# Kernel optimization log

Hardware: AMD Instinct MI355X
Metric: run time of the kernel (lower is better)

## Reference

```python
import jax, jax.numpy as jnp
import numpy as np

DIS_NORM = 6.0 * 512 / 1000.0  # 6 * D(z=0) * Nmesh / Boxsize with D(0)=1


def setup_inputs() -> dict:
    key = jax.random.key(0)
    x = jax.random.normal(key, (2, 4, 128, 128, 128), dtype=jnp.float32)
    return {"x": x}


def _lag2eul(x):
    N, C = x.shape[0], x.shape[1]
    D, H, W = x.shape[2], x.shape[3], x.shape[4]
    P = D * H * W
    Cout = C - 3 if C > 3 else 1

    # rm_dis_mean=True: mean displacement, detached
    dis_mean = jax.lax.stop_gradient(jnp.mean(x[:, :3], axis=(2, 3, 4), keepdims=True))

    pos = (x[:, :3] - dis_mean) * DIS_NORM  # (N,3,D,H,W)
    gd = jnp.arange(D, dtype=x.dtype) + 0.5
    gh = jnp.arange(H, dtype=x.dtype) + 0.5
    gw = jnp.arange(W, dtype=x.dtype) + 0.5
    grid = jnp.stack(jnp.meshgrid(gd, gh, gw, indexing='ij'))  # (3,D,H,W)
    pos = (pos + grid[None]).reshape(N, 3, P)

    if C > 3:
        val = x[:, 3:].reshape(N, Cout, P)
    else:
        val = jnp.ones((N, Cout, P), dtype=x.dtype)

    intpos = jnp.floor(pos).astype(jnp.int32)
    # 8 trilinear neighbors: bit b of n -> offset along dim b
    neighbors = (jnp.arange(8, dtype=jnp.int32)[None, :] >> jnp.arange(3, dtype=jnp.int32)[:, None]) & 1  # (3,8)
    tgt = intpos[:, :, :, None] + neighbors[None, :, None, :]  # (N,3,P,8)

    kernel = jnp.prod(1.0 - jnp.abs(pos[:, :, :, None] - tgt.astype(x.dtype)), axis=1)  # (N,P,8)
    src = val[:, :, :, None] * kernel[:, None, :, :]  # (N,Cout,P,8)

    # periodic=False: mask out-of-bounds deposits
    bounds = jnp.array([D, H, W], dtype=jnp.int32)[None, :, None, None]
    mask = jnp.all((tgt >= 0) & (tgt < bounds), axis=1)  # (N,P,8)
    ind = (tgt[:, 0] * H + tgt[:, 1]) * W + tgt[:, 2]  # (N,P,8)
    ind = jnp.clip(ind, 0, P - 1)
    src = jnp.where(mask[:, None, :, :], src, jnp.zeros((), dtype=x.dtype))

    def scatter_one(ind_n, src_n):
        mesh = jnp.zeros((Cout, P), dtype=src_n.dtype)
        return mesh.at[:, ind_n.reshape(-1)].add(src_n.reshape(Cout, -1))

    mesh = jax.vmap(scatter_one)(ind, src)  # (N,Cout,P)
    return mesh.reshape(N, Cout, D, H, W)


def reference(x):
    return _lag2eul(x)
```

## Files before the change

### kernel.cpp

```cpp
#include <hip/hip_runtime.h>

#define NBATCH 2
#define NDIM   128
#define NP     (128 * 128 * 128)
#define DIS_NORM 3.072f

#define TS   16
#define LO   5
#define HI   6
#define WIN  (TS + LO + HI)
#define WIN2 (WIN * WIN)
#define WINF (WIN * WIN * WIN)
#define TPB  8
#define NTILE (TPB * TPB * TPB)
#define NTHR 512

#define FXSCALE 16777216.0f
#define FXINV   (1.0f / 16777216.0f)

#define SLAB 19696

#define SUMS_OFF 0
#define SLABS_OFF 1024
#define WS_FLOATS ((size_t)SLABS_OFF + (size_t)NBATCH * NTILE * SLAB)
#define WS_NEEDED_BYTES (WS_FLOATS * sizeof(float))

__device__ __constant__ int BASE27[27] = {
    0,216,792,972,1548,3084,3564,3744,4224,
    4376,4952,6488,6968,8504,12600,13880,14360,15640,
    16040,16220,16700,16852,17332,18612,19012,19164,19564};

__global__ __launch_bounds__(256) void prep_kernel(const float* __restrict__ x,
                                                   float* __restrict__ ws,
                                                   float* __restrict__ out) {
    const int plane = blockIdx.y;
    if (plane < 6) {
        const int n = plane / 3, c = plane % 3;
        const float4* xp = (const float4*)(x + ((size_t)n * 4 + c) * NP);
        float s = 0.0f;
        for (int i = blockIdx.x * 256 + threadIdx.x; i < NP / 4; i += 128 * 256) {
            float4 v = xp[i];
            s += (v.x + v.y) + (v.z + v.w);
        }
        #pragma unroll
        for (int off = 32; off > 0; off >>= 1) s += __shfl_down(s, off, 64);
        __shared__ float wsum[4];
        if ((threadIdx.x & 63) == 0) wsum[threadIdx.x >> 6] = s;
        __syncthreads();
        if (threadIdx.x == 0)
            ws[SUMS_OFF + plane * 128 + blockIdx.x] =
                (wsum[0] + wsum[1]) + (wsum[2] + wsum[3]);
    } else {
        float4* o4 = (float4*)out;
        const float4 z = make_float4(0.f, 0.f, 0.f, 0.f);
        for (int i = blockIdx.x * 256 + threadIdx.x; i < NBATCH * NP / 4; i += 128 * 256)
            o4[i] = z;
    }
}

__device__ __forceinline__ void load_means128(const float* __restrict__ ws, int n,
                                              float& m0, float& m1, float& m2) {
    float s0 = 0.f, s1 = 0.f, s2 = 0.f;
    const float* p0 = ws + SUMS_OFF + (n * 3 + 0) * 128;
    const float* p1 = ws + SUMS_OFF + (n * 3 + 1) * 128;
    const float* p2 = ws + SUMS_OFF + (n * 3 + 2) * 128;
    #pragma unroll 4
    for (int b = 0; b < 128; ++b) { s0 += p0[b]; s1 += p1[b]; s2 += p2[b]; }
    const float inv_np = 1.0f / (float)NP;
    m0 = s0 * inv_np; m1 = s1 * inv_np; m2 = s2 * inv_np;
}

__device__ __forceinline__ void deposit_pair(unsigned long long* __restrict__ winU,
                                             int b, float va, float vb) {
    const int fa = __float2int_rn(va * FXSCALE);
    const int fb = __float2int_rn(vb * FXSCALE);
    const bool odd = (b & 1);
    const long long packed = (((long long)fb) << 32) + (long long)fa;
    const long long hiOnly = ((long long)fa) << 32;
    atomicAdd(&winU[b >> 1], (unsigned long long)(odd ? hiOnly : packed));
    if (odd) atomicAdd(&winU[(b >> 1) + 1], (unsigned long long)(long long)fb);
}

__global__ __launch_bounds__(NTHR, 4) void scatter_tile_kernel(
        const float* __restrict__ x, const float* __restrict__ ws,
        float* __restrict__ slabs, float* __restrict__ out) {
    const int blk = blockIdx.x;
    const int n = blk >> 9;
    const int t = blk & (NTILE - 1);
    const int tx = t & 7, ty = (t >> 3) & 7, tz = t >> 6;

    __shared__ ulonglong2 win2[(WINF + 3) / 4 + 1];
    unsigned long long* winU = (unsigned long long*)win2;
    {
        float4* z4 = (float4*)win2;
        const float4 z = make_float4(0.f, 0.f, 0.f, 0.f);
        for (int i = threadIdx.x; i < (WINF + 3) / 4 + 1; i += NTHR) z4[i] = z;
    }
    float m0, m1, m2;
    load_means128(ws, n, m0, m1, m2);
    __syncthreads();

    const int i0 = threadIdx.x * 8;
    const int lw0 = i0 & 15;
    const int lh  = (i0 >> 4) & 15;
    const int ld  = i0 >> 8;
    const int gd = tz * TS + ld, gh = ty * TS + lh, gw0 = tx * TS + lw0;
    const size_t prow = ((size_t)gd * NDIM + gh) * NDIM + gw0;

    const float4* x4 = (const float4*)(x + (size_t)n * 4 * NP);
    const size_t q = prow >> 2;
    const size_t s4 = NP / 4;
    float4 a0 = x4[0 * s4 + q], a1 = x4[0 * s4 + q + 1];
    float4 b0 = x4[1 * s4 + q], b1 = x4[1 * s4 + q + 1];
    float4 c0 = x4[2 * s4 + q], c1 = x4[2 * s4 + q + 1];
    float4 e0 = x4[3 * s4 + q], e1 = x4[3 * s4 + q + 1];
    const float D0[8] = {a0.x, a0.y, a0.z, a0.w, a1.x, a1.y, a1.z, a1.w};
    const float D1[8] = {b0.x, b0.y, b0.z, b0.w, b1.x, b1.y, b1.z, b1.w};
    const float D2[8] = {c0.x, c0.y, c0.z, c0.w, c1.x, c1.y, c1.z, c1.w};
    const float VV[8] = {e0.x, e0.y, e0.z, e0.w, e1.x, e1.y, e1.z, e1.w};

    const int od = tz * TS - LO, oh = ty * TS - LO, ow = tx * TS - LO;
    float* sp = out + (size_t)n * NP;

    #pragma unroll
    for (int k = 0; k < 8; ++k) {
        const float pd = (D0[k] - m0) * DIS_NORM + (float)gd + 0.5f;
        const float ph = (D1[k] - m1) * DIS_NORM + (float)gh + 0.5f;
        const float pw = (D2[k] - m2) * DIS_NORM + (float)(gw0 + k) + 0.5f;
        const float v = VV[k];

        const float fd = floorf(pd), fh = floorf(ph), fw = floorf(pw);
        const int id = (int)fd, ih = (int)fh, iw = (int)fw;
        const float rd = pd - fd, rh = ph - fh, rw = pw - fw;

        const int wd = id - od, wh = ih - oh, ww = iw - ow;
        if ((unsigned)wd <= WIN - 2 && (unsigned)wh <= WIN - 2 &&
            (unsigned)ww <= WIN - 2) {
            const int b00 = (wd * WIN + wh) * WIN + ww;
            const float sd0 = v * (1.0f - rd), sd1 = v * rd;
            const float h0 = 1.0f - rh, h1 = rh;
            const float q0 = 1.0f - rw, q1 = rw;
            deposit_pair(winU, b00,              sd0 * h0 * q0, sd0 * h0 * q1);
            deposit_pair(winU, b00 + WIN,        sd0 * h1 * q0, sd0 * h1 * q1);
            deposit_pair(winU, b00 + WIN2,       sd1 * h0 * q0, sd1 * h0 * q1);
            deposit_pair(winU, b00 + WIN2 + WIN, sd1 * h1 * q0, sd1 * h1 * q1);
        } else {
            const float wd2[2]  = {1.0f - rd, rd};
            const float wh2[2]  = {1.0f - rh, rh};
            const float ww2[2]  = {1.0f - rw, rw};
            #pragma unroll
            for (int dd = 0; dd < 2; ++dd) {
                const int td = id + dd, wdc = wd + dd;
                const bool dW = (unsigned)wdc < WIN, dM = (unsigned)td < NDIM;
                if (!dM && !dW) continue;
                #pragma unroll
                for (int hh = 0; hh < 2; ++hh) {
                    const int th = ih + hh, whc = wh + hh;
                    const bool hW = (unsigned)whc < WIN, hM = (unsigned)th < NDIM;
                    const float vdh = v * wd2[dd] * wh2[hh];
                    #pragma unroll
                    for (int wi = 0; wi < 2; ++wi) {
                        const int tw = iw + wi, wwc = ww + wi;
                        const bool wW = (unsigned)wwc < WIN, wM = (unsigned)tw < NDIM;
                        const float dep = vdh * ww2[wi];
                        if (dW && hW && wW) {
                            const int cb = (wdc * WIN + whc) * WIN + wwc;
                            const int fx = __float2int_rn(dep * FXSCALE);
                            const long long cv = (cb & 1)
                                ? (((long long)fx) << 32) : (long long)fx;
                            atomicAdd(&winU[cb >> 1], (unsigned long long)cv);
                        } else if (dM && hM && wM) {
                            atomicAdd(sp + ((size_t)td * NDIM + th) * NDIM + tw, dep);
                        }
                    }
                }
            }
        }
    }

    __syncthreads();

    {
        const int NU = (WINF + 1) / 2;
        for (int i = threadIdx.x; i < NU; i += NTHR) {
            const unsigned long long u = winU[i];
            const int lo = (int)(unsigned)(u & 0xffffffffull);
            const int hi = (int)(u >> 32) + (lo < 0 ? 1 : 0);
            float2 f;
            f.x = (float)lo * FXINV;
            f.y = (float)hi * FXINV;
            ((float2*)winU)[i] = f;
        }
    }
    __syncthreads();
    const float* winF = (const float*)winU;

    const int EXTY[3] = {6, 16, 5};
    const int nbase = n << 9;
    for (int r = threadIdx.x; r < WIN2; r += NTHR) {
        const int lz = r / WIN;
        const int ly = r - lz * WIN;
        int mz, pz;
        if (lz < LO) { mz = -1; pz = lz; }
        else if (lz < LO + TS) { mz = 0; pz = lz - LO; }
        else { mz = 1; pz = lz - LO - TS; }
        int my, py;
        if (ly < LO) { my = -1; py = ly; }
        else if (ly < LO + TS) { my = 0; py = ly - LO; }
        else { my = 1; py = ly - LO - TS; }
        const int dtz = tz + mz, dty = ty + my;
        if ((unsigned)dtz >= TPB || (unsigned)dty >= TPB) continue;

        const int jz = 1 - mz, jy = 1 - my;
        const int ey = EXTY[jy];
        const int rowoff = pz * ey + py;
        const int pobase = jz * 9 + jy * 3;
        const float* src = winF + r * WIN;
        const int slabRow = nbase + (dtz * 8 + dty) * 8;

        if (tx > 0) {
            float* d = slabs + (size_t)(slabRow + tx - 1) * SLAB
                     + BASE27[pobase + 2] + rowoff * 5;
            #pragma unroll
            for (int k = 0; k < 5; ++k) d[k] = src[k];
        }
        {
            float* d = slabs + (size_t)(slabRow + tx) * SLAB
                     + BASE27[pobase + 1] + rowoff * 16;
            #pragma unroll
            for (int k = 0; k < 4; ++k) {
                float4 v;
                v.x = src[5 + 4 * k]; v.y = src[6 + 4 * k];
                v.z = src[7 + 4 * k]; v.w = src[8 + 4 * k];
                ((float4*)d)[k] = v;
            }
        }
        if (tx < TPB - 1) {
            float* d = slabs + (size_t)(slabRow + tx + 1) * SLAB
                     + BASE27[pobase + 0] + rowoff * 6;
            #pragma unroll
            for (int k = 0; k < 6; ++k) d[k] = src[21 + k];
        }
    }
}

__global__ __launch_bounds__(NTHR) void gather_tile_kernel(const float* __restrict__ slabs,
                                                           float* __restrict__ out) {
    const int blk = blockIdx.x;
    const int t = blk & (NTILE - 1);
    const int tx = t & 7, ty = (t >> 3) & 7, tz = t >> 6;

    __shared__ float tile[TS * TS * TS];
    for (int i = threadIdx.x; i < TS * TS * TS; i += NTHR) tile[i] = 0.0f;
    __syncthreads();

    const float* slab = slabs + (size_t)blk * SLAB;
    const int EXT[3] = {6, 16, 5};
    const int DST[3] = {0, 0, 11};

    #pragma unroll
    for (int sec = 0; sec < 27; ++sec) {
        const int jz = sec / 9, jy = (sec / 3) % 3, jx = sec % 3;
        const int oz = jz - 1, oy = jy - 1, ox = jx - 1;
        if ((unsigned)(tz + oz) < TPB && (unsigned)(ty + oy) < TPB &&
            (unsigned)(tx + ox) < TPB) {
            const int ez = EXT[jz], ey = EXT[jy], ex = EXT[jx];
            const int sz = DST[jz], sy = DST[jy], sx = DST[jx];
            const float* pc = slab + BASE27[sec];
            if (jx == 1) {
                const int nq = ez * ey * 4;
                for (int i4 = threadIdx.x; i4 < nq; i4 += NTHR) {
                    const int row = i4 >> 2, qd = i4 & 3;
                    const int pz = row / ey, py = row - pz * ey;
                    float4 v = ((const float4*)pc)[i4];
                    float4* tp = (float4*)&tile[((sz + pz) * TS + sy + py) * TS + qd * 4];
                    float4 o = *tp;
                    o.x += v.x; o.y += v.y; o.z += v.z; o.w += v.w;
                    *tp = o;
                }
            } else {
                const int npc = ez * ey * ex;
                for (int i = threadIdx.x; i < npc; i += NTHR) {
                    const int pz = i / (ey * ex);
                    const int r  = i - pz * (ey * ex);
                    const int py = r / ex;
                    const int px = r - py * ex;
                    tile[((sz + pz) * TS + sy + py) * TS + sx + px] += pc[i];
                }
            }
        }
        __syncthreads();
    }

    const int n = blk >> 9;
    float* ob = out + (size_t)n * NP;
    for (int i4 = threadIdx.x; i4 < TS * TS * TS / 4; i4 += NTHR) {
        const int xq = i4 & 3, y = (i4 >> 2) & 15, z = i4 >> 6;
        float4 v = ((const float4*)tile)[i4];
        const size_t g = (((size_t)(tz * TS + z) * NDIM) + ty * TS + y) * NDIM
                       + tx * TS + xq * 4;
        float4 o = *(const float4*)(ob + g);
        v.x += o.x; v.y += o.y; v.z += o.z; v.w += o.w;
        *(float4*)(ob + g) = v;
    }
}

__global__ __launch_bounds__(256) void scatter_direct_kernel(const float* __restrict__ x,
                                                             const float* __restrict__ ws,
                                                             float* __restrict__ out) {
    const int lin = blockIdx.x * 256 + threadIdx.x;
    const int n = lin >> 21;
    const int p = lin & (NP - 1);

    float m0, m1, m2;
    load_means128(ws, n, m0, m1, m2);

    const size_t base = (size_t)n * 4 * NP;
    const float d0 = x[base + 0 * (size_t)NP + p];
    const float d1 = x[base + 1 * (size_t)NP + p];
    const float d2 = x[base + 2 * (size_t)NP + p];
    const float v  = x[base + 3 * (size_t)NP + p];

    const int w = p & 127, h = (p >> 7) & 127, d = p >> 14;
    const float pd = (d0 - m0) * DIS_NORM + (float)d + 0.5f;
    const float ph = (d1 - m1) * DIS_NORM + (float)h + 0.5f;
    const float pw = (d2 - m2) * DIS_NORM + (float)w + 0.5f;
    const float fd = floorf(pd), fh = floorf(ph), fw = floorf(pw);
    const int id = (int)fd, ih = (int)fh, iw = (int)fw;
    const float rd = pd - fd, rh = ph - fh, rw = pw - fw;
    const float wd[2] = {1.0f - rd, rd}, wh[2] = {1.0f - rh, rh}, ww[2] = {1.0f - rw, rw};
    float* o = out + (size_t)n * NP;
    #pragma unroll
    for (int dd = 0; dd < 2; ++dd) {
        const int td = id + dd;
        if ((unsigned)td >= (unsigned)NDIM) continue;
        #pragma unroll
        for (int hh = 0; hh < 2; ++hh) {
            const int th = ih + hh;
            if ((unsigned)th >= (unsigned)NDIM) continue;
            const float vdh = v * wd[dd] * wh[hh];
            const int rowbase = (td * NDIM + th) * NDIM;
            #pragma unroll
            for (int wi = 0; wi < 2; ++wi) {
                const int tw = iw + wi;
                if ((unsigned)tw >= (unsigned)NDIM) continue;
                atomicAdd(o + rowbase + tw, vdh * ww[wi]);
            }
        }
    }
}

extern "C" void kernel_launch(void* const* d_in, const int* in_sizes, int n_in,
                              void* d_out, int out_size, void* d_ws, size_t ws_size,
                              hipStream_t stream) {
    const float* x = (const float*)d_in[0];
    float* out = (float*)d_out;
    float* ws = (float*)d_ws;
    float* slabs = ws + SLABS_OFF;

    dim3 pgrid(128, 7);

    if (ws_size >= WS_NEEDED_BYTES) {
        prep_kernel<<<pgrid, 256, 0, stream>>>(x, ws, out);
        scatter_tile_kernel<<<dim3(NBATCH * NTILE), NTHR, 0, stream>>>(x, ws, slabs, out);
        gather_tile_kernel<<<dim3(NBATCH * NTILE), NTHR, 0, stream>>>(slabs, out);
    } else {
        prep_kernel<<<pgrid, 256, 0, stream>>>(x, ws, out);
        scatter_direct_kernel<<<dim3(NBATCH * NP / 256), 256, 0, stream>>>(x, ws, out);
    }
}
```

Before: 187.6 us.

## Queue out-of-window particles for a second pass and gather slabs per-voxel

In the scatter kernel, particles whose neighbourhood falls outside the fast window are appended to a shared-memory queue instead of taking the divergent slow branch inline. After a barrier, the whole block reprocesses the queued particles by re-reading x from global memory, which is meant to reduce warp divergence in the main loop. The gather kernel drops the shared tile and its 27 sync-separated section passes. Each thread now sums up to eight slab contributions for its voxel directly and adds the result to the output with scalar rather than float4 accesses.

```diff
diff --git a/kernel.cpp b/kernel.cpp
--- a/kernel.cpp
+++ b/kernel.cpp
@@ -17,6 +17,8 @@
 
 #define FXSCALE 16777216.0f
 #define FXINV   (1.0f / 16777216.0f)
+
+#define QCAP 1280
 
 #define SLAB 19696
 
@@ -81,6 +83,46 @@
     if (odd) atomicAdd(&winU[(b >> 1) + 1], (unsigned long long)(long long)fb);
 }
 
+__device__ __forceinline__ void slow_deposit(unsigned long long* __restrict__ winU,
+                                             float* __restrict__ sp,
+                                             float pd, float ph, float pw, float v,
+                                             int od, int oh, int ow) {
+    const float fd = floorf(pd), fh = floorf(ph), fw = floorf(pw);
+    const int id = (int)fd, ih = (int)fh, iw = (int)fw;
+    const float rd = pd - fd, rh = ph - fh, rw = pw - fw;
+    const int wd = id - od, wh = ih - oh, ww = iw - ow;
+    const float wd2[2] = {1.0f - rd, rd};
+    const float wh2[2] = {1.0f - rh, rh};
+    const float ww2[2] = {1.0f - rw, rw};
+    #pragma unroll
+    for (int dd = 0; dd < 2; ++dd) {
+        const int td = id + dd, wdc = wd + dd;
+        const bool dW = (unsigned)wdc < WIN, dM = (unsigned)td < NDIM;
+        if (!dM && !dW) continue;
+        #pragma unroll
+        for (int hh = 0; hh < 2; ++hh) {
+            const int th = ih + hh, whc = wh + hh;
+            const bool hW = (unsigned)whc < WIN, hM = (unsigned)th < NDIM;
+            const float vdh = v * wd2[dd] * wh2[hh];
+            #pragma unroll
+            for (int wi = 0; wi < 2; ++wi) {
+                const int tw = iw + wi, wwc = ww + wi;
+                const bool wW = (unsigned)wwc < WIN, wM = (unsigned)tw < NDIM;
+                const float dep = vdh * ww2[wi];
+                if (dW && hW && wW) {
+                    const int cb = (wdc * WIN + whc) * WIN + wwc;
+                    const int fx = __float2int_rn(dep * FXSCALE);
+                    const long long cv = (cb & 1)
+                        ? (((long long)fx) << 32) : (long long)fx;
+                    atomicAdd(&winU[cb >> 1], (unsigned long long)cv);
+                } else if (dM && hM && wM) {
+                    atomicAdd(sp + ((size_t)td * NDIM + th) * NDIM + tw, dep);
+                }
+            }
+        }
+    }
+}
+
 __global__ __launch_bounds__(NTHR, 4) void scatter_tile_kernel(
         const float* __restrict__ x, const float* __restrict__ ws,
         float* __restrict__ slabs, float* __restrict__ out) {
@@ -90,11 +132,14 @@
     const int tx = t & 7, ty = (t >> 3) & 7, tz = t >> 6;
 
     __shared__ ulonglong2 win2[(WINF + 3) / 4 + 1];
+    __shared__ int qcount;
+    __shared__ unsigned short queue[QCAP];
     unsigned long long* winU = (unsigned long long*)win2;
     {
         float4* z4 = (float4*)win2;
         const float4 z = make_float4(0.f, 0.f, 0.f, 0.f);
         for (int i = threadIdx.x; i < (WINF + 3) / 4 + 1; i += NTHR) z4[i] = z;
+        if (threadIdx.x == 0) qcount = 0;
     }
     float m0, m1, m2;
     load_means128(ws, n, m0, m1, m2);
@@ -145,39 +190,32 @@
             deposit_pair(winU, b00 + WIN2,       sd1 * h0 * q0, sd1 * h0 * q1);
             deposit_pair(winU, b00 + WIN2 + WIN, sd1 * h1 * q0, sd1 * h1 * q1);
         } else {
-            const float wd2[2]  = {1.0f - rd, rd};
-            const float wh2[2]  = {1.0f - rh, rh};
-            const float ww2[2]  = {1.0f - rw, rw};
-            #pragma unroll
-            for (int dd = 0; dd < 2; ++dd) {
-                const int td = id + dd, wdc = wd + dd;
-                const bool dW = (unsigned)wdc < WIN, dM = (unsigned)td < NDIM;
-                if (!dM && !dW) continue;
-                #pragma unroll
-                for (int hh = 0; hh < 2; ++hh) {
-                    const int th = ih + hh, whc = wh + hh;
-                    const bool hW = (unsigned)whc < WIN, hM = (unsigned)th < NDIM;
-                    const float vdh = v * wd2[dd] * wh2[hh];
-                    #pragma unroll
-                    for (int wi = 0; wi < 2; ++wi) {
-                        const int tw = iw + wi, wwc = ww + wi;
-                        const bool wW = (unsigned)wwc < WIN, wM = (unsigned)tw < NDIM;
-                        const float dep = vdh * ww2[wi];
-                        if (dW && hW && wW) {
-                            const int cb = (wdc * WIN + whc) * WIN + wwc;
-                            const int fx = __float2int_rn(dep * FXSCALE);
-                            const long long cv = (cb & 1)
-                                ? (((long long)fx) << 32) : (long long)fx;
-                            atomicAdd(&winU[cb >> 1], (unsigned long long)cv);
-                        } else if (dM && hM && wM) {
-                            atomicAdd(sp + ((size_t)td * NDIM + th) * NDIM + tw, dep);
-                        }
-                    }
-                }
-            }
-        }
-    }
-
+            const int qi = atomicAdd(&qcount, 1);
+            if (qi < QCAP) {
+                queue[qi] = (unsigned short)(i0 + k);
+            } else {
+                slow_deposit(winU, sp, pd, ph, pw, v, od, oh, ow);
+            }
+        }
+    }
+
+    __syncthreads();
+
+    {
+        const int nq = min(qcount, QCAP);
+        const float* xb = x + (size_t)n * 4 * NP;
+        for (int qi = threadIdx.x; qi < nq; qi += NTHR) {
+            const int p = queue[qi];
+            const int lw = p & 15, lhq = (p >> 4) & 15, ldq = p >> 8;
+            const int gdq = tz * TS + ldq, ghq = ty * TS + lhq, gwq = tx * TS + lw;
+            const size_t pr = ((size_t)gdq * NDIM + ghq) * NDIM + gwq;
+            const float pd = (xb[pr] - m0) * DIS_NORM + (float)gdq + 0.5f;
+            const float ph = (xb[(size_t)NP + pr] - m1) * DIS_NORM + (float)ghq + 0.5f;
+            const float pw = (xb[2 * (size_t)NP + pr] - m2) * DIS_NORM + (float)gwq + 0.5f;
+            const float v = xb[3 * (size_t)NP + pr];
+            slow_deposit(winU, sp, pd, ph, pw, v, od, oh, ow);
+        }
+    }
     __syncthreads();
 
     {
@@ -247,61 +285,44 @@
 __global__ __launch_bounds__(NTHR) void gather_tile_kernel(const float* __restrict__ slabs,
                                                            float* __restrict__ out) {
     const int blk = blockIdx.x;
+    const int n = blk >> 9;
     const int t = blk & (NTILE - 1);
     const int tx = t & 7, ty = (t >> 3) & 7, tz = t >> 6;
 
-    __shared__ float tile[TS * TS * TS];
-    for (int i = threadIdx.x; i < TS * TS * TS; i += NTHR) tile[i] = 0.0f;
-    __syncthreads();
-
-    const float* slab = slabs + (size_t)blk * SLAB;
-    const int EXT[3] = {6, 16, 5};
-    const int DST[3] = {0, 0, 11};
-
-    #pragma unroll
-    for (int sec = 0; sec < 27; ++sec) {
-        const int jz = sec / 9, jy = (sec / 3) % 3, jx = sec % 3;
-        const int oz = jz - 1, oy = jy - 1, ox = jx - 1;
-        if ((unsigned)(tz + oz) < TPB && (unsigned)(ty + oy) < TPB &&
-            (unsigned)(tx + ox) < TPB) {
-            const int ez = EXT[jz], ey = EXT[jy], ex = EXT[jx];
-            const int sz = DST[jz], sy = DST[jy], sx = DST[jx];
-            const float* pc = slab + BASE27[sec];
-            if (jx == 1) {
-                const int nq = ez * ey * 4;
-                for (int i4 = threadIdx.x; i4 < nq; i4 += NTHR) {
-                    const int row = i4 >> 2, qd = i4 & 3;
-                    const int pz = row / ey, py = row - pz * ey;
-                    float4 v = ((const float4*)pc)[i4];
-                    float4* tp = (float4*)&tile[((sz + pz) * TS + sy + py) * TS + qd * 4];
-                    float4 o = *tp;
-                    o.x += v.x; o.y += v.y; o.z += v.z; o.w += v.w;
-                    *tp = o;
-                }
-            } else {
-                const int npc = ez * ey * ex;
-                for (int i = threadIdx.x; i < npc; i += NTHR) {
-                    const int pz = i / (ey * ex);
-                    const int r  = i - pz * (ey * ex);
-                    const int py = r / ex;
-                    const int px = r - py * ex;
-                    tile[((sz + pz) * TS + sy + py) * TS + sx + px] += pc[i];
-                }
-            }
-        }
-        __syncthreads();
-    }
-
-    const int n = blk >> 9;
-    float* ob = out + (size_t)n * NP;
-    for (int i4 = threadIdx.x; i4 < TS * TS * TS / 4; i4 += NTHR) {
-        const int xq = i4 & 3, y = (i4 >> 2) & 15, z = i4 >> 6;
-        float4 v = ((const float4*)tile)[i4];
+    const float* __restrict__ slab = slabs + (size_t)blk * SLAB;
+    float* __restrict__ ob = out + (size_t)n * NP;
+
+    for (int i = threadIdx.x; i < TS * TS * TS; i += NTHR) {
+        const int x = i & 15, y = (i >> 4) & 15, z = i >> 8;
+
+        int zt2 = 0, zp2 = 0, ze2 = 0; bool z2 = false;
+        if (z < 6)        { if (tz > 0)       { zt2 = 0;  zp2 = z;      ze2 = 6; z2 = true; } }
+        else if (z >= 11) { if (tz < TPB - 1) { zt2 = 18; zp2 = z - 11; ze2 = 5; z2 = true; } }
+        int yt2 = 0, yp2 = 0, ye2 = 0; bool y2 = false;
+        if (y < 6)        { if (ty > 0)       { yt2 = 0;  yp2 = y;      ye2 = 6; y2 = true; } }
+        else if (y >= 11) { if (ty < TPB - 1) { yt2 = 6;  yp2 = y - 11; ye2 = 5; y2 = true; } }
+        int xt2 = 0, xp2 = 0, xe2 = 0; bool x2 = false;
+        if (x < 6)        { if (tx > 0)       { xt2 = 0;  xp2 = x;      xe2 = 6; x2 = true; } }
+        else if (x >= 11) { if (tx < TPB - 1) { xt2 = 2;  xp2 = x - 11; xe2 = 5; x2 = true; } }
+
+        float s = slab[BASE27[13] + (z * 16 + y) * 16 + x];
+        if (x2) s += slab[BASE27[9 + 3 + xt2] + (z * 16 + y) * xe2 + xp2];
+        if (y2) {
+            s += slab[BASE27[9 + yt2 + 1] + (z * ye2 + yp2) * 16 + x];
+            if (x2) s += slab[BASE27[9 + yt2 + xt2] + (z * ye2 + yp2) * xe2 + xp2];
+        }
+        if (z2) {
+            s += slab[BASE27[zt2 + 3 + 1] + (zp2 * 16 + y) * 16 + x];
+            if (x2) s += slab[BASE27[zt2 + 3 + xt2] + (zp2 * 16 + y) * xe2 + xp2];
+            if (y2) {
+                s += slab[BASE27[zt2 + yt2 + 1] + (zp2 * ye2 + yp2) * 16 + x];
+                if (x2) s += slab[BASE27[zt2 + yt2 + xt2] + (zp2 * ye2 + yp2) * xe2 + xp2];
+            }
+        }
+
         const size_t g = (((size_t)(tz * TS + z) * NDIM) + ty * TS + y) * NDIM
-                       + tx * TS + xq * 4;
-        float4 o = *(const float4*)(ob + g);
-        v.x += o.x; v.y += o.y; v.z += o.z; v.w += o.w;
-        *(float4*)(ob + g) = v;
+                       + tx * TS + x;
+        ob[g] += s;
     }
 }
 
```

New measurement: 198.6 us. 5.9% more time.
